# Kernel tuning notes

Measured on AMD Instinct MI355X. Metric: run time of the kernel, lower is better.

The kernel has to match this reference:

```python
import jax, jax.numpy as jnp
import numpy as np

VOCAB = 50000
EMB = 200        # embedding_size
CAP = 3          # capitalization_size
IN = EMB + CAP   # LSTM input size = 203
HID = 128        # LSTMCell(128)
B = 256
T = 500          # comment_length
NC = 6           # num_classes
DENSE = 64


def _lstm_scan(x_tbi, W, b):
    """x_tbi: [T,B,IN]. W: [IN+HID, 4*HID] (tf gate order i, j, f, o), b: [4*HID].
    Returns h sequence [T,B,HID]. forget_bias=1.0 as in tf.contrib.rnn.LSTMCell."""
    h0 = jnp.zeros((x_tbi.shape[1], HID), x_tbi.dtype)

    def step(carry, x):
        h, c = carry
        gates = jnp.concatenate([x, h], axis=-1) @ W + b   # [B, 4*HID]
        i, j, f, o = jnp.split(gates, 4, axis=-1)
        c = jax.nn.sigmoid(f + 1.0) * c + jax.nn.sigmoid(i) * jnp.tanh(j)
        h = jax.nn.sigmoid(o) * jnp.tanh(c)
        return (h, c), h

    _, hs = jax.lax.scan(step, (h0, h0), x_tbi)
    return hs


def setup_inputs() -> dict:
    key = jax.random.key(0)
    ks = jax.random.split(key, 12)
    words = jax.random.randint(ks[0], (B, T), 0, VOCAB, dtype=jnp.int32)
    capitals = jax.random.randint(ks[1], (B, T), 0, CAP, dtype=jnp.int32)
    # word embeddings: random trainable table with a trailing zero-padding row
    word_emb = jax.random.normal(ks[2], (VOCAB + 1, EMB), dtype=jnp.float32) * 0.1
    # capitalization embedding: one_hot_embedding_matrix(3) = [eye(3); zeros(1,3)]
    cap_emb = jnp.concatenate([jnp.eye(CAP, dtype=jnp.float32),
                               jnp.zeros((1, CAP), dtype=jnp.float32)], axis=0)
    def glorot(k, shape):
        lim = np.sqrt(6.0 / (shape[0] + shape[1]))
        return jax.random.uniform(k, shape, jnp.float32, -lim, lim)
    W_fw = glorot(ks[3], (IN + HID, 4 * HID))
    b_fw = jnp.zeros((4 * HID,), jnp.float32)
    W_bw = glorot(ks[4], (IN + HID, 4 * HID))
    b_bw = jnp.zeros((4 * HID,), jnp.float32)
    W1 = glorot(ks[5], (2 * HID, DENSE))
    b1 = jnp.zeros((DENSE,), jnp.float32)
    W2 = glorot(ks[6], (DENSE, NC))
    b2 = jnp.zeros((NC,), jnp.float32)
    return {"words": words, "capitals": capitals, "word_emb": word_emb,
            "cap_emb": cap_emb, "W_fw": W_fw, "b_fw": b_fw,
            "W_bw": W_bw, "b_bw": b_bw, "W1": W1, "b1": b1,
            "W2": W2, "b2": b2}


def reference(words, capitals, word_emb, cap_emb, W_fw, b_fw, W_bw, b_bw,
              W1, b1, W2, b2):
    # embedding lookups and concat -> [B, T, 203]
    x = jnp.concatenate([word_emb[words], cap_emb[capitals]], axis=-1)
    x_tbi = jnp.transpose(x, (1, 0, 2))                    # [T, B, IN]
    # forward direction: take output at last timestep
    h_fw_last = _lstm_scan(x_tbi, W_fw, b_fw)[-1]          # [B, HID]
    # backward direction: bidirectional_dynamic_rnn reverses bw outputs back,
    # so outputs[1][:, 0, :] == last state of scan over the reversed sequence
    h_bw_first = _lstm_scan(x_tbi[::-1], W_bw, b_bw)[-1]   # [B, HID]
    rnn_output = jnp.concatenate([h_fw_last, h_bw_first], axis=1)  # [B, 256]
    dense1 = jax.nn.elu(rnn_output @ W1 + b1)              # [B, 64]
    y_hat = jax.nn.sigmoid(dense1 @ W2 + b2)               # [B, NC]
    return y_hat
```

## Files before the change

### kernel.cpp

```cpp
#include <hip/hip_runtime.h>

#define T 500
#define NB 256
#define VROWS 50001
#define EMB 200
#define KPAD 224
#define MPAD 50048
#define LOG2E 1.44269504f

typedef unsigned short u16;
typedef __attribute__((ext_vector_type(8))) __bf16 bf16x8;
typedef __attribute__((ext_vector_type(8))) short short8;
typedef __attribute__((ext_vector_type(4))) float f32x4;
typedef __attribute__((ext_vector_type(4))) u16 u16x4;
typedef __attribute__((ext_vector_type(4))) int i32x4;

__device__ __forceinline__ u16 f2bf(float x) {
  __bf16 h = (__bf16)x;
  return __builtin_bit_cast(u16, h);
}
__device__ __forceinline__ float bf2f(u16 b) {
  union { unsigned u; float f; } v; v.u = ((unsigned)b) << 16;
  return v.f;
}
__device__ __forceinline__ float rcp_(float x) { return __builtin_amdgcn_rcpf(x); }
__device__ __forceinline__ float ex2_(float x) { return __builtin_amdgcn_exp2f(x); }
__device__ __forceinline__ float gsc(int g) { return (g == 1) ? 2.f * LOG2E : -LOG2E; }

__global__ void prep_kernel(const int* __restrict__ words, const int* __restrict__ caps,
                            const float* __restrict__ word_emb,
                            const float* __restrict__ cap_emb,
                            const float* __restrict__ Wfw, const float* __restrict__ bfw,
                            const float* __restrict__ Wbw, const float* __restrict__ bbw,
                            int* __restrict__ wordsT, int* __restrict__ capsT,
                            float* __restrict__ Cproj, u16* __restrict__ Apad,
                            u16* __restrict__ Bt) {
  const int S0 = NB * T;
  const int S1 = MPAD * (KPAD / 4);
  const int S2 = 2 * 512 * KPAD;
  const int S3 = 2 * 4 * 512;
  int tid = blockIdx.x * blockDim.x + threadIdx.x;
  int nthr = gridDim.x * blockDim.x;
  for (int i = tid; i < S0 + S1 + S2 + S3; i += nthr) {
    if (i < S0) {
      int b = i / T, t = i - b * T;
      wordsT[t * NB + b] = words[i];
      capsT[t * NB + b]  = caps[i];
    } else if (i < S0 + S1) {
      int idx = i - S0;
      int v = idx / (KPAD / 4), q = idx - v * (KPAD / 4);
      int k = q * 4;
      u16x4 o;
      if (v < VROWS && k < EMB) {
        const float* p = word_emb + (size_t)v * EMB + k;
        o[0] = f2bf(p[0]); o[1] = f2bf(p[1]); o[2] = f2bf(p[2]); o[3] = f2bf(p[3]);
      } else {
        o[0] = o[1] = o[2] = o[3] = 0;
      }
      *(u16x4*)(Apad + (size_t)v * KPAD + k) = o;
    } else if (i < S0 + S1 + S2) {
      int idx = i - S0 - S1;
      int d = idx / (512 * KPAD), rem = idx - d * (512 * KPAD);
      int colp = rem / KPAD, k = rem - colp * KPAD;
      const float* W = d ? Wbw : Wfw;
      int g = colp & 3, jj = colp >> 2;
      Bt[idx] = (k < EMB) ? f2bf(W[k * 512 + g * 128 + jj] * gsc(g)) : (u16)0;
    } else {
      int idx = i - S0 - S1 - S2;
      int dir = idx >> 11; int c = (idx >> 9) & 3; int colp = idx & 511;
      int j = colp >> 2, g = colp & 3;
      const float* W = dir ? Wbw : Wfw;
      const float* bias = dir ? bbw : bfw;
      float v = bias[g * 128 + j] + (g == 2 ? 1.f : 0.f);
      #pragma unroll
      for (int cc = 0; cc < 3; ++cc)
        v += cap_emb[c * 3 + cc] * W[(200 + cc) * 512 + g * 128 + j];
      Cproj[idx] = v * gsc(g);
    }
  }
}

__global__ __launch_bounds__(256) void vproj_kernel(
    const u16* __restrict__ Apad, const u16* __restrict__ Bt,
    u16* __restrict__ Vfw, u16* __restrict__ Vbw) {
  const int mt = blockIdx.x, nt = blockIdx.y, dir = blockIdx.z;
  const u16* __restrict__ B = Bt + (size_t)dir * 512 * KPAD;
  u16* __restrict__ V = dir ? Vbw : Vfw;

  __shared__ u16 Al[2][128 * 32];
  __shared__ u16 Bl[2][128 * 32];

  const int tid = threadIdx.x;
  const int w = tid >> 6, l = tid & 63;
  const int la = l & 15, lb = l >> 4;
  const int m0 = mt * 128, n0 = nt * 128;

  auto stage = [&](int buf, int ks) {
    int k0 = ks * 32;
    #pragma unroll
    for (int h = 0; h < 2; ++h) {
      int c = w * 128 + h * 64 + l;
      int row = c >> 2, kq = c & 3;
      const u16* ga = Apad + (size_t)(m0 + row) * KPAD + k0 + kq * 8;
      __builtin_amdgcn_global_load_lds(
          (const __attribute__((address_space(1))) void*)ga,
          (__attribute__((address_space(3))) void*)&Al[buf][(w * 128 + h * 64) * 8],
          16, 0, 0);
      const u16* gb = B + (size_t)(n0 + row) * KPAD + k0 + kq * 8;
      __builtin_amdgcn_global_load_lds(
          (const __attribute__((address_space(1))) void*)gb,
          (__attribute__((address_space(3))) void*)&Bl[buf][(w * 128 + h * 64) * 8],
          16, 0, 0);
    }
  };

  f32x4 z = {0.f, 0.f, 0.f, 0.f};
  f32x4 acc[4][4] = {{z,z,z,z},{z,z,z,z},{z,z,z,z},{z,z,z,z}};
  const int wr = w >> 1, wc = w & 1;

  stage(0, 0);
  __syncthreads();
  #pragma unroll 1
  for (int ks = 0; ks < 7; ++ks) {
    int cur = ks & 1;
    if (ks < 6) stage(cur ^ 1, ks + 1);
    bf16x8 af[4], bfr[4];
    #pragma unroll
    for (int m = 0; m < 4; ++m)
      af[m] = *(const bf16x8*)&Al[cur][(wr * 64 + m * 16 + la) * 32 + lb * 8];
    #pragma unroll
    for (int n = 0; n < 4; ++n)
      bfr[n] = *(const bf16x8*)&Bl[cur][(wc * 64 + n * 16 + la) * 32 + lb * 8];
    #pragma unroll
    for (int m = 0; m < 4; ++m)
      #pragma unroll
      for (int n = 0; n < 4; ++n)
        acc[m][n] = __builtin_amdgcn_mfma_f32_16x16x32_bf16(af[m], bfr[n], acc[m][n], 0, 0, 0);
    __syncthreads();
  }

  #pragma unroll
  for (int m = 0; m < 4; ++m) {
    #pragma unroll
    for (int n = 0; n < 4; ++n) {
      #pragma unroll
      for (int r = 0; r < 4; ++r) {
        int v = m0 + wr * 64 + m * 16 + lb * 4 + r;
        int colp = n0 + wc * 64 + n * 16 + la;
        V[(size_t)v * 512 + colp] = f2bf(acc[m][n][r]);
      }
    }
  }
}

template <int PAR>
__device__ __forceinline__ void lstm_step(
    int t, int dir, int b0, int la, int lb, int j,
    const int* __restrict__ wordsT, const int* __restrict__ capsT,
    const u16* __restrict__ V, const float* __restrict__ Cp,
    const bf16x8 (&bfrag)[4][4], u16* __restrict__ hbuf,
    u16x4 (&vw_c)[4], f32x4 (&cp_c)[4],
    i32x4& wi_c, i32x4& ci_c,
    i32x4& wi_g, i32x4& ci_g,
    u16x4 (&vw_g)[4], f32x4 (&cp_g)[4],
    f32x4& cst, f32x4& hl) {
  {
    int ts = t + 4; if (ts > T - 1) ts = T - 1;
    int tt = dir ? (T - 1 - ts) : ts;
    wi_c = *(const i32x4*)(wordsT + tt * NB + b0 + lb * 4);
    ci_c = *(const i32x4*)(capsT + tt * NB + b0 + lb * 4);
  }
  #pragma unroll
  for (int r = 0; r < 4; ++r) {
    vw_g[r] = *(const u16x4*)(V + (size_t)wi_g[r] * 512 + j * 4);
    cp_g[r] = *(const f32x4*)(Cp + ci_g[r] * 512 + j * 4);
  }

  const u16* hb = hbuf + PAR * 2048;
  const int swz = (la & 7) << 3;
  bf16x8 afr[4];
  #pragma unroll
  for (int kk = 0; kk < 4; ++kk)
    afr[kk] = *(const bf16x8*)(hb + ((la * 128 + kk * 32 + lb * 8) ^ swz));

  f32x4 acc0, acc1, acc2, acc3;
  #pragma unroll
  for (int r = 0; r < 4; ++r) {
    acc0[r] = bf2f(vw_c[r][0]) + cp_c[r][0];
    acc1[r] = bf2f(vw_c[r][1]) + cp_c[r][1];
    acc2[r] = bf2f(vw_c[r][2]) + cp_c[r][2];
    acc3[r] = bf2f(vw_c[r][3]) + cp_c[r][3];
  }
  #pragma unroll
  for (int kk = 0; kk < 4; ++kk) {
    acc0 = __builtin_amdgcn_mfma_f32_16x16x32_bf16(afr[kk], bfrag[0][kk], acc0, 0, 0, 0);
    acc1 = __builtin_amdgcn_mfma_f32_16x16x32_bf16(afr[kk], bfrag[1][kk], acc1, 0, 0, 0);
    acc2 = __builtin_amdgcn_mfma_f32_16x16x32_bf16(afr[kk], bfrag[2][kk], acc2, 0, 0, 0);
    acc3 = __builtin_amdgcn_mfma_f32_16x16x32_bf16(afr[kk], bfrag[3][kk], acc3, 0, 0, 0);
  }
  u16* ho = hbuf + (PAR ^ 1) * 2048;
  #pragma unroll
  for (int r = 0; r < 4; ++r) {
    float ig = rcp_(1.f + ex2_(acc0[r]));
    float tj = 1.f - 2.f * rcp_(1.f + ex2_(acc1[r]));
    float fg = rcp_(1.f + ex2_(acc2[r]));
    float cn = fg * cst[r] + ig * tj;
    cst[r] = cn;
    float og = rcp_(1.f + ex2_(acc3[r]));
    float hn = og * (1.f - 2.f * rcp_(1.f + ex2_(2.f * LOG2E * cn)));
    hl[r] = hn;
    int row = lb * 4 + r;
    ho[(row * 128 + j) ^ ((row & 7) << 3)] = f2bf(hn);
  }
  __builtin_amdgcn_sched_barrier(0);
  asm volatile("s_waitcnt lgkmcnt(0)");
  __builtin_amdgcn_s_barrier();
  __builtin_amdgcn_sched_barrier(0);
}

__global__ __launch_bounds__(512, 1) void lstm_kernel(
    const int* __restrict__ wordsT, const int* __restrict__ capsT,
    const u16* __restrict__ Vfw, const u16* __restrict__ Vbw,
    const float* __restrict__ CprojAll, const float* __restrict__ Wfw,
    const float* __restrict__ Wbw, float* __restrict__ rnn) {
  const int dir = blockIdx.x & 1;
  const int chunk = blockIdx.x >> 1;
  const int b0 = chunk * 16;
  const u16* __restrict__ V = dir ? Vbw : Vfw;
  const float* __restrict__ Cp = CprojAll + dir * 4 * 512;
  const float* __restrict__ W = dir ? Wbw : Wfw;

  const int tid = threadIdx.x;
  const int w = tid >> 6, l = tid & 63, la = l & 15, lb = l >> 4;
  const int j = w * 16 + la;

  bf16x8 bfrag[4][4];
  #pragma unroll
  for (int g = 0; g < 4; ++g) {
    #pragma unroll
    for (int kk = 0; kk < 4; ++kk) {
      short8 t8;
      #pragma unroll
      for (int r = 0; r < 8; ++r) {
        int k = kk * 32 + lb * 8 + r;
        t8[r] = (short)f2bf(W[(203 + k) * 512 + g * 128 + j] * gsc(g));
      }
      bfrag[g][kk] = __builtin_bit_cast(bf16x8, t8);
    }
  }

  __shared__ u16 hbuf[2 * 16 * 128];
  for (int i = tid; i < 2 * 16 * 128; i += 512) hbuf[i] = 0;

  f32x4 cst = {0.f, 0.f, 0.f, 0.f};
  f32x4 hl  = {0.f, 0.f, 0.f, 0.f};

  i32x4 wiA, ciA, wiB, ciB, wiC, ciC, wiD, ciD;
  u16x4 vwA[4], vwB[4], vwC[4], vwD[4];
  f32x4 cpA[4], cpB[4], cpC[4], cpD[4];
  {
    int t0 = dir ? (T - 1) : 0;
    int t1 = dir ? (T - 2) : 1;
    int t2 = dir ? (T - 3) : 2;
    int t3 = dir ? (T - 4) : 3;
    wiA = *(const i32x4*)(wordsT + t0 * NB + b0 + lb * 4);
    ciA = *(const i32x4*)(capsT + t0 * NB + b0 + lb * 4);
    wiB = *(const i32x4*)(wordsT + t1 * NB + b0 + lb * 4);
    ciB = *(const i32x4*)(capsT + t1 * NB + b0 + lb * 4);
    wiC = *(const i32x4*)(wordsT + t2 * NB + b0 + lb * 4);
    ciC = *(const i32x4*)(capsT + t2 * NB + b0 + lb * 4);
    wiD = *(const i32x4*)(wordsT + t3 * NB + b0 + lb * 4);
    ciD = *(const i32x4*)(capsT + t3 * NB + b0 + lb * 4);
  }
  #pragma unroll
  for (int r = 0; r < 4; ++r) {
    vwA[r] = *(const u16x4*)(V + (size_t)wiA[r] * 512 + j * 4);
    cpA[r] = *(const f32x4*)(Cp + ciA[r] * 512 + j * 4);
    vwB[r] = *(const u16x4*)(V + (size_t)wiB[r] * 512 + j * 4);
    cpB[r] = *(const f32x4*)(Cp + ciB[r] * 512 + j * 4);
  }
  __syncthreads();

  #pragma unroll 1
  for (int tq = 0; tq < T / 4; ++tq) {
    int t0 = 4 * tq;
    lstm_step<0>(t0,     dir, b0, la, lb, j, wordsT, capsT, V, Cp, bfrag, hbuf,
                 vwA, cpA, wiA, ciA, wiC, ciC, vwC, cpC, cst, hl);
    lstm_step<1>(t0 + 1, dir, b0, la, lb, j, wordsT, capsT, V, Cp, bfrag, hbuf,
                 vwB, cpB, wiB, ciB, wiD, ciD, vwD, cpD, cst, hl);
    lstm_step<0>(t0 + 2, dir, b0, la, lb, j, wordsT, capsT, V, Cp, bfrag, hbuf,
                 vwC, cpC, wiC, ciC, wiA, ciA, vwA, cpA, cst, hl);
    lstm_step<1>(t0 + 3, dir, b0, la, lb, j, wordsT, capsT, V, Cp, bfrag, hbuf,
                 vwD, cpD, wiD, ciD, wiB, ciB, vwB, cpB, cst, hl);
  }

  #pragma unroll
  for (int r = 0; r < 4; ++r)
    rnn[(size_t)(b0 + lb * 4 + r) * 256 + dir * 128 + j] = hl[r];
}

__global__ void head_kernel(const float* __restrict__ rnn, const float* __restrict__ W1,
                            const float* __restrict__ b1, const float* __restrict__ W2,
                            const float* __restrict__ b2, float* __restrict__ out) {
  int b = blockIdx.x;
  int jj = threadIdx.x;
  __shared__ float d1[64];
  float acc = b1[jj];
  const float* r = rnn + b * 256;
  #pragma unroll 4
  for (int k = 0; k < 256; ++k) acc += r[k] * W1[k * 64 + jj];
  d1[jj] = acc > 0.f ? acc : (__expf(acc) - 1.f);
  __syncthreads();
  if (jj < 6) {
    float a2 = b2[jj];
    #pragma unroll 8
    for (int k = 0; k < 64; ++k) a2 += d1[k] * W2[k * 6 + jj];
    out[b * 6 + jj] = rcp_(1.f + __expf(-a2));
  }
}

extern "C" void kernel_launch(void* const* d_in, const int* in_sizes, int n_in,
                              void* d_out, int out_size, void* d_ws, size_t ws_size,
                              hipStream_t stream) {
  (void)in_sizes; (void)n_in; (void)out_size; (void)ws_size;
  const int*   words    = (const int*)  d_in[0];
  const int*   caps     = (const int*)  d_in[1];
  const float* word_emb = (const float*)d_in[2];
  const float* cap_emb  = (const float*)d_in[3];
  const float* Wfw      = (const float*)d_in[4];
  const float* bfw      = (const float*)d_in[5];
  const float* Wbw      = (const float*)d_in[6];
  const float* bbw      = (const float*)d_in[7];
  const float* W1       = (const float*)d_in[8];
  const float* b1       = (const float*)d_in[9];
  const float* W2       = (const float*)d_in[10];
  const float* b2       = (const float*)d_in[11];
  float* out = (float*)d_out;

  char* base = (char*)d_ws;
  size_t off = 0;
  auto alloc = [&](size_t bytes) {
    char* q = base + off;
    off = (off + bytes + 255) & ~(size_t)255;
    return q;
  };
  u16*   Vfw    = (u16*)  alloc((size_t)MPAD * 512 * 2);
  u16*   Vbw    = (u16*)  alloc((size_t)MPAD * 512 * 2);
  u16*   Apad   = (u16*)  alloc((size_t)MPAD * KPAD * 2);
  u16*   Bt     = (u16*)  alloc((size_t)2 * 512 * KPAD * 2);
  int*   wordsT = (int*)  alloc((size_t)T * NB * 4);
  int*   capsT  = (int*)  alloc((size_t)T * NB * 4);
  float* Cproj  = (float*)alloc((size_t)2 * 4 * 512 * 4);
  float* rnn    = (float*)alloc((size_t)256 * 256 * 4);

  hipLaunchKernelGGL(prep_kernel, dim3(2048), dim3(256), 0, stream,
                     words, caps, word_emb, cap_emb, Wfw, bfw, Wbw, bbw,
                     wordsT, capsT, Cproj, Apad, Bt);
  hipLaunchKernelGGL(vproj_kernel, dim3(MPAD / 128, 4, 2), dim3(256), 0, stream,
                     Apad, Bt, Vfw, Vbw);
  hipLaunchKernelGGL(lstm_kernel, dim3(32), dim3(512), 0, stream,
                     wordsT, capsT, Vfw, Vbw, Cproj, Wfw, Wbw, rnn);
  hipLaunchKernelGGL(head_kernel, dim3(256), dim3(64), 0, stream,
                     rnn, W1, b1, W2, b2, out);
}
```

Before: 580.0 us.

## Halve LSTM block to 4 waves, each computing two 16-column hidden slices

The recurrent LSTM kernel now runs 256 threads (4 waves) per block instead of 512 (8 waves). Each wave handles 32 hidden units as two 16-column groups, with doubled MFMA accumulators, weight fragments and prefetch registers. The goal is to cut the per-step block barrier cost and give each wave more independent MFMA work to hide latency. In exchange, register pressure per thread roughly doubles and the gate math per wave is serialised over twice as many elements.

```diff
diff --git a/kernel.cpp b/kernel.cpp
--- a/kernel.cpp
+++ b/kernel.cpp
@@ -155,15 +155,22 @@
 
 template <int PAR>
 __device__ __forceinline__ void lstm_step(
-    int t, int dir, int b0, int la, int lb, int j,
+    int t, int dir, int b0, int la, int lb, int w,
     const int* __restrict__ wordsT, const int* __restrict__ capsT,
     const u16* __restrict__ V, const float* __restrict__ Cp,
-    const bf16x8 (&bfrag)[4][4], u16* __restrict__ hbuf,
-    u16x4 (&vw_c)[4], f32x4 (&cp_c)[4],
+    const bf16x8 (&bfrag)[4][2][4], u16* __restrict__ hbuf,
+    u16x4 (&vw_c)[2][4], f32x4 (&cp_c)[2][4],
     i32x4& wi_c, i32x4& ci_c,
     i32x4& wi_g, i32x4& ci_g,
-    u16x4 (&vw_g)[4], f32x4 (&cp_g)[4],
-    f32x4& cst, f32x4& hl) {
+    u16x4 (&vw_g)[2][4], f32x4 (&cp_g)[2][4],
+    f32x4 (&cst)[2], f32x4 (&hl)[2]) {
+  const u16* hb = hbuf + PAR * 2048;
+  const int swz = (la & 7) << 3;
+  bf16x8 afr[4];
+  #pragma unroll
+  for (int kk = 0; kk < 4; ++kk)
+    afr[kk] = *(const bf16x8*)(hb + ((la * 128 + kk * 32 + lb * 8) ^ swz));
+
   {
     int ts = t + 4; if (ts > T - 1) ts = T - 1;
     int tt = dir ? (T - 1 - ts) : ts;
@@ -171,54 +178,58 @@
     ci_c = *(const i32x4*)(capsT + tt * NB + b0 + lb * 4);
   }
   #pragma unroll
-  for (int r = 0; r < 4; ++r) {
-    vw_g[r] = *(const u16x4*)(V + (size_t)wi_g[r] * 512 + j * 4);
-    cp_g[r] = *(const f32x4*)(Cp + ci_g[r] * 512 + j * 4);
-  }
-
-  const u16* hb = hbuf + PAR * 2048;
-  const int swz = (la & 7) << 3;
-  bf16x8 afr[4];
+  for (int jg = 0; jg < 2; ++jg) {
+    int jc = w * 32 + jg * 16 + la;
+    #pragma unroll
+    for (int r = 0; r < 4; ++r) {
+      vw_g[jg][r] = *(const u16x4*)(V + (size_t)wi_g[r] * 512 + jc * 4);
+      cp_g[jg][r] = *(const f32x4*)(Cp + ci_g[r] * 512 + jc * 4);
+    }
+  }
+
+  f32x4 acc[4][2];
+  #pragma unroll
+  for (int jg = 0; jg < 2; ++jg)
+    #pragma unroll
+    for (int r = 0; r < 4; ++r) {
+      acc[0][jg][r] = bf2f(vw_c[jg][r][0]) + cp_c[jg][r][0];
+      acc[1][jg][r] = bf2f(vw_c[jg][r][1]) + cp_c[jg][r][1];
+      acc[2][jg][r] = bf2f(vw_c[jg][r][2]) + cp_c[jg][r][2];
+      acc[3][jg][r] = bf2f(vw_c[jg][r][3]) + cp_c[jg][r][3];
+    }
   #pragma unroll
   for (int kk = 0; kk < 4; ++kk)
-    afr[kk] = *(const bf16x8*)(hb + ((la * 128 + kk * 32 + lb * 8) ^ swz));
-
-  f32x4 acc0, acc1, acc2, acc3;
-  #pragma unroll
-  for (int r = 0; r < 4; ++r) {
-    acc0[r] = bf2f(vw_c[r][0]) + cp_c[r][0];
-    acc1[r] = bf2f(vw_c[r][1]) + cp_c[r][1];
-    acc2[r] = bf2f(vw_c[r][2]) + cp_c[r][2];
-    acc3[r] = bf2f(vw_c[r][3]) + cp_c[r][3];
-  }
-  #pragma unroll
-  for (int kk = 0; kk < 4; ++kk) {
-    acc0 = __builtin_amdgcn_mfma_f32_16x16x32_bf16(afr[kk], bfrag[0][kk], acc0, 0, 0, 0);
-    acc1 = __builtin_amdgcn_mfma_f32_16x16x32_bf16(afr[kk], bfrag[1][kk], acc1, 0, 0, 0);
-    acc2 = __builtin_amdgcn_mfma_f32_16x16x32_bf16(afr[kk], bfrag[2][kk], acc2, 0, 0, 0);
-    acc3 = __builtin_amdgcn_mfma_f32_16x16x32_bf16(afr[kk], bfrag[3][kk], acc3, 0, 0, 0);
-  }
+    #pragma unroll
+    for (int g = 0; g < 4; ++g)
+      #pragma unroll
+      for (int jg = 0; jg < 2; ++jg)
+        acc[g][jg] = __builtin_amdgcn_mfma_f32_16x16x32_bf16(
+            afr[kk], bfrag[g][jg][kk], acc[g][jg], 0, 0, 0);
+
   u16* ho = hbuf + (PAR ^ 1) * 2048;
   #pragma unroll
-  for (int r = 0; r < 4; ++r) {
-    float ig = rcp_(1.f + ex2_(acc0[r]));
-    float tj = 1.f - 2.f * rcp_(1.f + ex2_(acc1[r]));
-    float fg = rcp_(1.f + ex2_(acc2[r]));
-    float cn = fg * cst[r] + ig * tj;
-    cst[r] = cn;
-    float og = rcp_(1.f + ex2_(acc3[r]));
-    float hn = og * (1.f - 2.f * rcp_(1.f + ex2_(2.f * LOG2E * cn)));
-    hl[r] = hn;
-    int row = lb * 4 + r;
-    ho[(row * 128 + j) ^ ((row & 7) << 3)] = f2bf(hn);
-  }
+  for (int jg = 0; jg < 2; ++jg)
+    #pragma unroll
+    for (int r = 0; r < 4; ++r) {
+      float ig = rcp_(1.f + ex2_(acc[0][jg][r]));
+      float tj = 1.f - 2.f * rcp_(1.f + ex2_(acc[1][jg][r]));
+      float fg = rcp_(1.f + ex2_(acc[2][jg][r]));
+      float cn = fg * cst[jg][r] + ig * tj;
+      cst[jg][r] = cn;
+      float og = rcp_(1.f + ex2_(acc[3][jg][r]));
+      float hn = og * (1.f - 2.f * rcp_(1.f + ex2_(2.f * LOG2E * cn)));
+      hl[jg][r] = hn;
+      int row = lb * 4 + r;
+      int col = w * 32 + jg * 16 + la;
+      ho[(row * 128 + col) ^ ((row & 7) << 3)] = f2bf(hn);
+    }
   __builtin_amdgcn_sched_barrier(0);
   asm volatile("s_waitcnt lgkmcnt(0)");
   __builtin_amdgcn_s_barrier();
   __builtin_amdgcn_sched_barrier(0);
 }
 
-__global__ __launch_bounds__(512, 1) void lstm_kernel(
+__global__ __launch_bounds__(256, 1) void lstm_kernel(
     const int* __restrict__ wordsT, const int* __restrict__ capsT,
     const u16* __restrict__ Vfw, const u16* __restrict__ Vbw,
     const float* __restrict__ CprojAll, const float* __restrict__ Wfw,
@@ -232,32 +243,32 @@
 
   const int tid = threadIdx.x;
   const int w = tid >> 6, l = tid & 63, la = l & 15, lb = l >> 4;
-  const int j = w * 16 + la;
-
-  bf16x8 bfrag[4][4];
-  #pragma unroll
-  for (int g = 0; g < 4; ++g) {
-    #pragma unroll
-    for (int kk = 0; kk < 4; ++kk) {
-      short8 t8;
-      #pragma unroll
-      for (int r = 0; r < 8; ++r) {
-        int k = kk * 32 + lb * 8 + r;
-        t8[r] = (short)f2bf(W[(203 + k) * 512 + g * 128 + j] * gsc(g));
+
+  bf16x8 bfrag[4][2][4];
+  #pragma unroll
+  for (int g = 0; g < 4; ++g)
+    #pragma unroll
+    for (int jg = 0; jg < 2; ++jg)
+      #pragma unroll
+      for (int kk = 0; kk < 4; ++kk) {
+        short8 t8;
+        #pragma unroll
+        for (int r = 0; r < 8; ++r) {
+          int k = kk * 32 + lb * 8 + r;
+          t8[r] = (short)f2bf(W[(203 + k) * 512 + g * 128 + w * 32 + jg * 16 + la] * gsc(g));
+        }
+        bfrag[g][jg][kk] = __builtin_bit_cast(bf16x8, t8);
       }
-      bfrag[g][kk] = __builtin_bit_cast(bf16x8, t8);
-    }
-  }
 
   __shared__ u16 hbuf[2 * 16 * 128];
-  for (int i = tid; i < 2 * 16 * 128; i += 512) hbuf[i] = 0;
-
-  f32x4 cst = {0.f, 0.f, 0.f, 0.f};
-  f32x4 hl  = {0.f, 0.f, 0.f, 0.f};
+  for (int i = tid; i < 2 * 16 * 128; i += 256) hbuf[i] = 0;
+
+  f32x4 cst[2] = {{0.f,0.f,0.f,0.f},{0.f,0.f,0.f,0.f}};
+  f32x4 hl[2]  = {{0.f,0.f,0.f,0.f},{0.f,0.f,0.f,0.f}};
 
   i32x4 wiA, ciA, wiB, ciB, wiC, ciC, wiD, ciD;
-  u16x4 vwA[4], vwB[4], vwC[4], vwD[4];
-  f32x4 cpA[4], cpB[4], cpC[4], cpD[4];
+  u16x4 vwA[2][4], vwB[2][4], vwC[2][4], vwD[2][4];
+  f32x4 cpA[2][4], cpB[2][4], cpC[2][4], cpD[2][4];
   {
     int t0 = dir ? (T - 1) : 0;
     int t1 = dir ? (T - 2) : 1;
@@ -273,30 +284,36 @@
     ciD = *(const i32x4*)(capsT + t3 * NB + b0 + lb * 4);
   }
   #pragma unroll
-  for (int r = 0; r < 4; ++r) {
-    vwA[r] = *(const u16x4*)(V + (size_t)wiA[r] * 512 + j * 4);
-    cpA[r] = *(const f32x4*)(Cp + ciA[r] * 512 + j * 4);
-    vwB[r] = *(const u16x4*)(V + (size_t)wiB[r] * 512 + j * 4);
-    cpB[r] = *(const f32x4*)(Cp + ciB[r] * 512 + j * 4);
+  for (int jg = 0; jg < 2; ++jg) {
+    int jc = w * 32 + jg * 16 + la;
+    #pragma unroll
+    for (int r = 0; r < 4; ++r) {
+      vwA[jg][r] = *(const u16x4*)(V + (size_t)wiA[r] * 512 + jc * 4);
+      cpA[jg][r] = *(const f32x4*)(Cp + ciA[r] * 512 + jc * 4);
+      vwB[jg][r] = *(const u16x4*)(V + (size_t)wiB[r] * 512 + jc * 4);
+      cpB[jg][r] = *(const f32x4*)(Cp + ciB[r] * 512 + jc * 4);
+    }
   }
   __syncthreads();
 
   #pragma unroll 1
   for (int tq = 0; tq < T / 4; ++tq) {
     int t0 = 4 * tq;
-    lstm_step<0>(t0,     dir, b0, la, lb, j, wordsT, capsT, V, Cp, bfrag, hbuf,
+    lstm_step<0>(t0,     dir, b0, la, lb, w, wordsT, capsT, V, Cp, bfrag, hbuf,
                  vwA, cpA, wiA, ciA, wiC, ciC, vwC, cpC, cst, hl);
-    lstm_step<1>(t0 + 1, dir, b0, la, lb, j, wordsT, capsT, V, Cp, bfrag, hbuf,
+    lstm_step<1>(t0 + 1, dir, b0, la, lb, w, wordsT, capsT, V, Cp, bfrag, hbuf,
                  vwB, cpB, wiB, ciB, wiD, ciD, vwD, cpD, cst, hl);
-    lstm_step<0>(t0 + 2, dir, b0, la, lb, j, wordsT, capsT, V, Cp, bfrag, hbuf,
+    lstm_step<0>(t0 + 2, dir, b0, la, lb, w, wordsT, capsT, V, Cp, bfrag, hbuf,
                  vwC, cpC, wiC, ciC, wiA, ciA, vwA, cpA, cst, hl);
-    lstm_step<1>(t0 + 3, dir, b0, la, lb, j, wordsT, capsT, V, Cp, bfrag, hbuf,
+    lstm_step<1>(t0 + 3, dir, b0, la, lb, w, wordsT, capsT, V, Cp, bfrag, hbuf,
                  vwD, cpD, wiD, ciD, wiB, ciB, vwB, cpB, cst, hl);
   }
 
   #pragma unroll
-  for (int r = 0; r < 4; ++r)
-    rnn[(size_t)(b0 + lb * 4 + r) * 256 + dir * 128 + j] = hl[r];
+  for (int jg = 0; jg < 2; ++jg)
+    #pragma unroll
+    for (int r = 0; r < 4; ++r)
+      rnn[(size_t)(b0 + lb * 4 + r) * 256 + dir * 128 + w * 32 + jg * 16 + la] = hl[jg][r];
 }
 
 __global__ void head_kernel(const float* __restrict__ rnn, const float* __restrict__ W1,
@@ -358,7 +375,7 @@
                      wordsT, capsT, Cproj, Apad, Bt);
   hipLaunchKernelGGL(vproj_kernel, dim3(MPAD / 128, 4, 2), dim3(256), 0, stream,
                      Apad, Bt, Vfw, Vbw);
-  hipLaunchKernelGGL(lstm_kernel, dim3(32), dim3(512), 0, stream,
+  hipLaunchKernelGGL(lstm_kernel, dim3(32), dim3(256), 0, stream,
                      wordsT, capsT, Vfw, Vbw, Cproj, Wfw, Wbw, rnn);
   hipLaunchKernelGGL(head_kernel, dim3(256), dim3(64), 0, stream,
                      rnn, W1, b1, W2, b2, out);
```

Measured after the change: 743.8 us. +28.2%, slower.

## Project input per token instead of precomputing over whole vocabulary table

Applied to the files above, without the earlier changes.

Before, the input projection was precomputed for all 50k vocabulary rows and gathered inside the LSTM loop by word index. Now the GEMM runs over the B*T token sequence, gathering embeddings straight into LDS, adding the capitalization/bias term in the epilogue, and writing a time-major XP buffer. The recurrent kernel then streams contiguous per-step rows with a shorter prefetch distance, no index lookups, and raised wave priority around its MFMAs. Compute drops from 50k to 128k rows? Actually it rises (128k rows vs 50k), but the prep conversion of the whole table and the random gathers are removed, so the trade is more GEMM work for better locality and less prep.

```diff
diff --git a/kernel.cpp b/kernel.cpp
--- a/kernel.cpp
+++ b/kernel.cpp
@@ -5,15 +5,14 @@
 #define VROWS 50001
 #define EMB 200
 #define KPAD 224
-#define MPAD 50048
 #define LOG2E 1.44269504f
 
 typedef unsigned short u16;
 typedef __attribute__((ext_vector_type(8))) __bf16 bf16x8;
 typedef __attribute__((ext_vector_type(8))) short short8;
+typedef __attribute__((ext_vector_type(8))) u16 u16x8;
 typedef __attribute__((ext_vector_type(4))) float f32x4;
 typedef __attribute__((ext_vector_type(4))) u16 u16x4;
-typedef __attribute__((ext_vector_type(4))) int i32x4;
 
 __device__ __forceinline__ u16 f2bf(float x) {
   __bf16 h = (__bf16)x;
@@ -27,46 +26,23 @@
 __device__ __forceinline__ float ex2_(float x) { return __builtin_amdgcn_exp2f(x); }
 __device__ __forceinline__ float gsc(int g) { return (g == 1) ? 2.f * LOG2E : -LOG2E; }
 
-__global__ void prep_kernel(const int* __restrict__ words, const int* __restrict__ caps,
-                            const float* __restrict__ word_emb,
-                            const float* __restrict__ cap_emb,
+__global__ void prep_kernel(const float* __restrict__ cap_emb,
                             const float* __restrict__ Wfw, const float* __restrict__ bfw,
                             const float* __restrict__ Wbw, const float* __restrict__ bbw,
-                            int* __restrict__ wordsT, int* __restrict__ capsT,
-                            float* __restrict__ Cproj, u16* __restrict__ Apad,
-                            u16* __restrict__ Bt) {
-  const int S0 = NB * T;
-  const int S1 = MPAD * (KPAD / 4);
+                            float* __restrict__ Cproj, u16* __restrict__ Bt) {
   const int S2 = 2 * 512 * KPAD;
   const int S3 = 2 * 4 * 512;
   int tid = blockIdx.x * blockDim.x + threadIdx.x;
   int nthr = gridDim.x * blockDim.x;
-  for (int i = tid; i < S0 + S1 + S2 + S3; i += nthr) {
-    if (i < S0) {
-      int b = i / T, t = i - b * T;
-      wordsT[t * NB + b] = words[i];
-      capsT[t * NB + b]  = caps[i];
-    } else if (i < S0 + S1) {
-      int idx = i - S0;
-      int v = idx / (KPAD / 4), q = idx - v * (KPAD / 4);
-      int k = q * 4;
-      u16x4 o;
-      if (v < VROWS && k < EMB) {
-        const float* p = word_emb + (size_t)v * EMB + k;
-        o[0] = f2bf(p[0]); o[1] = f2bf(p[1]); o[2] = f2bf(p[2]); o[3] = f2bf(p[3]);
-      } else {
-        o[0] = o[1] = o[2] = o[3] = 0;
-      }
-      *(u16x4*)(Apad + (size_t)v * KPAD + k) = o;
-    } else if (i < S0 + S1 + S2) {
-      int idx = i - S0 - S1;
-      int d = idx / (512 * KPAD), rem = idx - d * (512 * KPAD);
+  for (int i = tid; i < S2 + S3; i += nthr) {
+    if (i < S2) {
+      int d = i / (512 * KPAD), rem = i - d * (512 * KPAD);
       int colp = rem / KPAD, k = rem - colp * KPAD;
       const float* W = d ? Wbw : Wfw;
       int g = colp & 3, jj = colp >> 2;
-      Bt[idx] = (k < EMB) ? f2bf(W[k * 512 + g * 128 + jj] * gsc(g)) : (u16)0;
+      Bt[i] = (k < EMB) ? f2bf(W[k * 512 + g * 128 + jj] * gsc(g)) : (u16)0;
     } else {
-      int idx = i - S0 - S1 - S2;
+      int idx = i - S2;
       int dir = idx >> 11; int c = (idx >> 9) & 3; int colp = idx & 511;
       int j = colp >> 2, g = colp & 3;
       const float* W = dir ? Wbw : Wfw;
@@ -80,36 +56,55 @@
   }
 }
 
-__global__ __launch_bounds__(256) void vproj_kernel(
-    const u16* __restrict__ Apad, const u16* __restrict__ Bt,
-    u16* __restrict__ Vfw, u16* __restrict__ Vbw) {
+__global__ __launch_bounds__(256) void xproj_kernel(
+    const int* __restrict__ words, const int* __restrict__ caps,
+    const float* __restrict__ word_emb, const u16* __restrict__ Bt,
+    const float* __restrict__ Cproj, u16* __restrict__ XP) {
   const int mt = blockIdx.x, nt = blockIdx.y, dir = blockIdx.z;
   const u16* __restrict__ B = Bt + (size_t)dir * 512 * KPAD;
-  u16* __restrict__ V = dir ? Vbw : Vfw;
-
-  __shared__ u16 Al[2][128 * 32];
-  __shared__ u16 Bl[2][128 * 32];
+  const float* __restrict__ Cb = Cproj + dir * 4 * 512;
+  u16* __restrict__ xp = XP + (size_t)dir * T * NB * 512;
+
+  __shared__ u16 As[2][128 * 32];
+  __shared__ u16 Bs[2][128 * 32];
 
   const int tid = threadIdx.x;
   const int w = tid >> 6, l = tid & 63;
   const int la = l & 15, lb = l >> 4;
   const int m0 = mt * 128, n0 = nt * 128;
-
-  auto stage = [&](int buf, int ks) {
+  const int tblk = m0 >> 8;
+
+  const int ar = tid >> 1, ah = tid & 1;
+  const int ab = (m0 & 255) + ar;
+  const int aword = words[ab * T + tblk];
+  const float* __restrict__ aemb = word_emb + (size_t)aword * EMB;
+
+  auto stageA = [&](int buf, int ks) {
+    int kbase = ks * 32 + ah * 16;
+    u16x8 lo, hi;
+    #pragma unroll
+    for (int q = 0; q < 4; ++q) {
+      int k = kbase + q * 4;
+      f32x4 v;
+      if (k < EMB) v = *(const f32x4*)(aemb + k);
+      else v = f32x4{0.f, 0.f, 0.f, 0.f};
+      u16 b0 = f2bf(v[0]), b1 = f2bf(v[1]), b2 = f2bf(v[2]), b3 = f2bf(v[3]);
+      if (q < 2) { lo[q*4+0]=b0; lo[q*4+1]=b1; lo[q*4+2]=b2; lo[q*4+3]=b3; }
+      else { int qq=q-2; hi[qq*4+0]=b0; hi[qq*4+1]=b1; hi[qq*4+2]=b2; hi[qq*4+3]=b3; }
+    }
+    *(u16x8*)&As[buf][ar * 32 + ah * 16]     = lo;
+    *(u16x8*)&As[buf][ar * 32 + ah * 16 + 8] = hi;
+  };
+  auto stageB = [&](int buf, int ks) {
     int k0 = ks * 32;
     #pragma unroll
     for (int h = 0; h < 2; ++h) {
       int c = w * 128 + h * 64 + l;
       int row = c >> 2, kq = c & 3;
-      const u16* ga = Apad + (size_t)(m0 + row) * KPAD + k0 + kq * 8;
-      __builtin_amdgcn_global_load_lds(
-          (const __attribute__((address_space(1))) void*)ga,
-          (__attribute__((address_space(3))) void*)&Al[buf][(w * 128 + h * 64) * 8],
-          16, 0, 0);
       const u16* gb = B + (size_t)(n0 + row) * KPAD + k0 + kq * 8;
       __builtin_amdgcn_global_load_lds(
           (const __attribute__((address_space(1))) void*)gb,
-          (__attribute__((address_space(3))) void*)&Bl[buf][(w * 128 + h * 64) * 8],
+          (__attribute__((address_space(3))) void*)&Bs[buf][(w * 128 + h * 64) * 8],
           16, 0, 0);
     }
   };
@@ -118,19 +113,19 @@
   f32x4 acc[4][4] = {{z,z,z,z},{z,z,z,z},{z,z,z,z},{z,z,z,z}};
   const int wr = w >> 1, wc = w & 1;
 
-  stage(0, 0);
+  stageA(0, 0); stageB(0, 0);
   __syncthreads();
   #pragma unroll 1
   for (int ks = 0; ks < 7; ++ks) {
     int cur = ks & 1;
-    if (ks < 6) stage(cur ^ 1, ks + 1);
+    if (ks < 6) { stageA(cur ^ 1, ks + 1); stageB(cur ^ 1, ks + 1); }
     bf16x8 af[4], bfr[4];
     #pragma unroll
     for (int m = 0; m < 4; ++m)
-      af[m] = *(const bf16x8*)&Al[cur][(wr * 64 + m * 16 + la) * 32 + lb * 8];
+      af[m] = *(const bf16x8*)&As[cur][(wr * 64 + m * 16 + la) * 32 + lb * 8];
     #pragma unroll
     for (int n = 0; n < 4; ++n)
-      bfr[n] = *(const bf16x8*)&Bl[cur][(wc * 64 + n * 16 + la) * 32 + lb * 8];
+      bfr[n] = *(const bf16x8*)&Bs[cur][(wc * 64 + n * 16 + la) * 32 + lb * 8];
     #pragma unroll
     for (int m = 0; m < 4; ++m)
       #pragma unroll
@@ -142,12 +137,15 @@
   #pragma unroll
   for (int m = 0; m < 4; ++m) {
     #pragma unroll
-    for (int n = 0; n < 4; ++n) {
+    for (int r = 0; r < 4; ++r) {
+      int b = (m0 & 255) + wr * 64 + m * 16 + lb * 4 + r;
+      int cap = caps[b * T + tblk];
+      const float* cbr = Cb + cap * 512;
+      u16* op = xp + ((size_t)tblk * NB + b) * 512;
       #pragma unroll
-      for (int r = 0; r < 4; ++r) {
-        int v = m0 + wr * 64 + m * 16 + lb * 4 + r;
+      for (int n = 0; n < 4; ++n) {
         int colp = n0 + wc * 64 + n * 16 + la;
-        V[(size_t)v * 512 + colp] = f2bf(acc[m][n][r]);
+        op[colp] = f2bf(acc[m][n][r] + cbr[colp]);
       }
     }
   }
@@ -155,27 +153,12 @@
 
 template <int PAR>
 __device__ __forceinline__ void lstm_step(
-    int t, int dir, int b0, int la, int lb, int j,
-    const int* __restrict__ wordsT, const int* __restrict__ capsT,
-    const u16* __restrict__ V, const float* __restrict__ Cp,
+    int t, int dir, int la, int lb, int j,
+    const u16* __restrict__ xpd, int voff0, int voff1, int voff2, int voff3,
     const bf16x8 (&bfrag)[4][4], u16* __restrict__ hbuf,
-    u16x4 (&vw_c)[4], f32x4 (&cp_c)[4],
-    i32x4& wi_c, i32x4& ci_c,
-    i32x4& wi_g, i32x4& ci_g,
-    u16x4 (&vw_g)[4], f32x4 (&cp_g)[4],
+    u16x4 (&xc)[4],
+    u16x4 (&xg)[4],
     f32x4& cst, f32x4& hl) {
-  {
-    int ts = t + 4; if (ts > T - 1) ts = T - 1;
-    int tt = dir ? (T - 1 - ts) : ts;
-    wi_c = *(const i32x4*)(wordsT + tt * NB + b0 + lb * 4);
-    ci_c = *(const i32x4*)(capsT + tt * NB + b0 + lb * 4);
-  }
-  #pragma unroll
-  for (int r = 0; r < 4; ++r) {
-    vw_g[r] = *(const u16x4*)(V + (size_t)wi_g[r] * 512 + j * 4);
-    cp_g[r] = *(const f32x4*)(Cp + ci_g[r] * 512 + j * 4);
-  }
-
   const u16* hb = hbuf + PAR * 2048;
   const int swz = (la & 7) << 3;
   bf16x8 afr[4];
@@ -183,14 +166,25 @@
   for (int kk = 0; kk < 4; ++kk)
     afr[kk] = *(const bf16x8*)(hb + ((la * 128 + kk * 32 + lb * 8) ^ swz));
 
+  {
+    int ts = t + 2; if (ts > T - 1) ts = T - 1;
+    int tt = dir ? (T - 1 - ts) : ts;
+    const u16* p = xpd + (size_t)tt * (NB * 512);
+    xg[0] = *(const u16x4*)(p + voff0);
+    xg[1] = *(const u16x4*)(p + voff1);
+    xg[2] = *(const u16x4*)(p + voff2);
+    xg[3] = *(const u16x4*)(p + voff3);
+  }
+
   f32x4 acc0, acc1, acc2, acc3;
   #pragma unroll
   for (int r = 0; r < 4; ++r) {
-    acc0[r] = bf2f(vw_c[r][0]) + cp_c[r][0];
-    acc1[r] = bf2f(vw_c[r][1]) + cp_c[r][1];
-    acc2[r] = bf2f(vw_c[r][2]) + cp_c[r][2];
-    acc3[r] = bf2f(vw_c[r][3]) + cp_c[r][3];
-  }
+    acc0[r] = bf2f(xc[r][0]);
+    acc1[r] = bf2f(xc[r][1]);
+    acc2[r] = bf2f(xc[r][2]);
+    acc3[r] = bf2f(xc[r][3]);
+  }
+  __builtin_amdgcn_s_setprio(1);
   #pragma unroll
   for (int kk = 0; kk < 4; ++kk) {
     acc0 = __builtin_amdgcn_mfma_f32_16x16x32_bf16(afr[kk], bfrag[0][kk], acc0, 0, 0, 0);
@@ -198,6 +192,7 @@
     acc2 = __builtin_amdgcn_mfma_f32_16x16x32_bf16(afr[kk], bfrag[2][kk], acc2, 0, 0, 0);
     acc3 = __builtin_amdgcn_mfma_f32_16x16x32_bf16(afr[kk], bfrag[3][kk], acc3, 0, 0, 0);
   }
+  __builtin_amdgcn_s_setprio(0);
   u16* ho = hbuf + (PAR ^ 1) * 2048;
   #pragma unroll
   for (int r = 0; r < 4; ++r) {
@@ -219,20 +214,22 @@
 }
 
 __global__ __launch_bounds__(512, 1) void lstm_kernel(
-    const int* __restrict__ wordsT, const int* __restrict__ capsT,
-    const u16* __restrict__ Vfw, const u16* __restrict__ Vbw,
-    const float* __restrict__ CprojAll, const float* __restrict__ Wfw,
+    const u16* __restrict__ XP, const float* __restrict__ Wfw,
     const float* __restrict__ Wbw, float* __restrict__ rnn) {
   const int dir = blockIdx.x & 1;
   const int chunk = blockIdx.x >> 1;
   const int b0 = chunk * 16;
-  const u16* __restrict__ V = dir ? Vbw : Vfw;
-  const float* __restrict__ Cp = CprojAll + dir * 4 * 512;
+  const u16* __restrict__ xpd = XP + (size_t)dir * T * NB * 512;
   const float* __restrict__ W = dir ? Wbw : Wfw;
 
   const int tid = threadIdx.x;
   const int w = tid >> 6, l = tid & 63, la = l & 15, lb = l >> 4;
   const int j = w * 16 + la;
+
+  const int voff0 = (b0 + lb * 4 + 0) * 512 + j * 4;
+  const int voff1 = (b0 + lb * 4 + 1) * 512 + j * 4;
+  const int voff2 = (b0 + lb * 4 + 2) * 512 + j * 4;
+  const int voff3 = (b0 + lb * 4 + 3) * 512 + j * 4;
 
   bf16x8 bfrag[4][4];
   #pragma unroll
@@ -255,43 +252,30 @@
   f32x4 cst = {0.f, 0.f, 0.f, 0.f};
   f32x4 hl  = {0.f, 0.f, 0.f, 0.f};
 
-  i32x4 wiA, ciA, wiB, ciB, wiC, ciC, wiD, ciD;
-  u16x4 vwA[4], vwB[4], vwC[4], vwD[4];
-  f32x4 cpA[4], cpB[4], cpC[4], cpD[4];
+  u16x4 xA[4], xB[4], xC[4], xD[4];
   {
-    int t0 = dir ? (T - 1) : 0;
-    int t1 = dir ? (T - 2) : 1;
-    int t2 = dir ? (T - 3) : 2;
-    int t3 = dir ? (T - 4) : 3;
-    wiA = *(const i32x4*)(wordsT + t0 * NB + b0 + lb * 4);
-    ciA = *(const i32x4*)(capsT + t0 * NB + b0 + lb * 4);
-    wiB = *(const i32x4*)(wordsT + t1 * NB + b0 + lb * 4);
-    ciB = *(const i32x4*)(capsT + t1 * NB + b0 + lb * 4);
-    wiC = *(const i32x4*)(wordsT + t2 * NB + b0 + lb * 4);
-    ciC = *(const i32x4*)(capsT + t2 * NB + b0 + lb * 4);
-    wiD = *(const i32x4*)(wordsT + t3 * NB + b0 + lb * 4);
-    ciD = *(const i32x4*)(capsT + t3 * NB + b0 + lb * 4);
-  }
-  #pragma unroll
-  for (int r = 0; r < 4; ++r) {
-    vwA[r] = *(const u16x4*)(V + (size_t)wiA[r] * 512 + j * 4);
-    cpA[r] = *(const f32x4*)(Cp + ciA[r] * 512 + j * 4);
-    vwB[r] = *(const u16x4*)(V + (size_t)wiB[r] * 512 + j * 4);
-    cpB[r] = *(const f32x4*)(Cp + ciB[r] * 512 + j * 4);
+    int tt0 = dir ? (T - 1) : 0;
+    int tt1 = dir ? (T - 2) : 1;
+    const u16* p0 = xpd + (size_t)tt0 * (NB * 512);
+    const u16* p1 = xpd + (size_t)tt1 * (NB * 512);
+    xA[0] = *(const u16x4*)(p0 + voff0); xA[1] = *(const u16x4*)(p0 + voff1);
+    xA[2] = *(const u16x4*)(p0 + voff2); xA[3] = *(const u16x4*)(p0 + voff3);
+    xB[0] = *(const u16x4*)(p1 + voff0); xB[1] = *(const u16x4*)(p1 + voff1);
+    xB[2] = *(const u16x4*)(p1 + voff2); xB[3] = *(const u16x4*)(p1 + voff3);
   }
   __syncthreads();
 
   #pragma unroll 1
   for (int tq = 0; tq < T / 4; ++tq) {
     int t0 = 4 * tq;
-    lstm_step<0>(t0,     dir, b0, la, lb, j, wordsT, capsT, V, Cp, bfrag, hbuf,
-                 vwA, cpA, wiA, ciA, wiC, ciC, vwC, cpC, cst, hl);
-    lstm_step<1>(t0 + 1, dir, b0, la, lb, j, wordsT, capsT, V, Cp, bfrag, hbuf,
-                 vwB, cpB, wiB, ciB, wiD, ciD, vwD, cpD, cst, hl);
-    lstm_step<0>(t0 + 2, dir, b0, la, lb, j, wordsT, capsT, V, Cp, bfrag, hbuf,
-                 vwC, cpC, wiC, ciC, wiA, ciA, vwA, cpA, cst, hl);
-    lstm_step<1>(t0 + 3, dir, b0, la, lb, j, wordsT, capsT, V, Cp, bfrag, hbuf,
-                 vwD, cpD, wiD, ciD, wiB, ciB, vwB, cpB, cst, hl);
+    lstm_step<0>(t0,     dir, la, lb, j, xpd, voff0, voff1, voff2, voff3,
+                 bfrag, hbuf, xA, xC, cst, hl);
+    lstm_step<1>(t0 + 1, dir, la, lb, j, xpd, voff0, voff1, voff2, voff3,
+                 bfrag, hbuf, xB, xD, cst, hl);
+    lstm_step<0>(t0 + 2, dir, la, lb, j, xpd, voff0, voff1, voff2, voff3,
+                 bfrag, hbuf, xC, xA, cst, hl);
+    lstm_step<1>(t0 + 3, dir, la, lb, j, xpd, voff0, voff1, voff2, voff3,
+                 bfrag, hbuf, xD, xB, cst, hl);
   }
 
   #pragma unroll
@@ -344,22 +328,17 @@
     off = (off + bytes + 255) & ~(size_t)255;
     return q;
   };
-  u16*   Vfw    = (u16*)  alloc((size_t)MPAD * 512 * 2);
-  u16*   Vbw    = (u16*)  alloc((size_t)MPAD * 512 * 2);
-  u16*   Apad   = (u16*)  alloc((size_t)MPAD * KPAD * 2);
+  u16*   XP     = (u16*)  alloc((size_t)2 * T * NB * 512 * 2);
   u16*   Bt     = (u16*)  alloc((size_t)2 * 512 * KPAD * 2);
-  int*   wordsT = (int*)  alloc((size_t)T * NB * 4);
-  int*   capsT  = (int*)  alloc((size_t)T * NB * 4);
   float* Cproj  = (float*)alloc((size_t)2 * 4 * 512 * 4);
   float* rnn    = (float*)alloc((size_t)256 * 256 * 4);
 
-  hipLaunchKernelGGL(prep_kernel, dim3(2048), dim3(256), 0, stream,
-                     words, caps, word_emb, cap_emb, Wfw, bfw, Wbw, bbw,
-                     wordsT, capsT, Cproj, Apad, Bt);
-  hipLaunchKernelGGL(vproj_kernel, dim3(MPAD / 128, 4, 2), dim3(256), 0, stream,
-                     Apad, Bt, Vfw, Vbw);
+  hipLaunchKernelGGL(prep_kernel, dim3(256), dim3(256), 0, stream,
+                     cap_emb, Wfw, bfw, Wbw, bbw, Cproj, Bt);
+  hipLaunchKernelGGL(xproj_kernel, dim3(1000, 4, 2), dim3(256), 0, stream,
+                     words, caps, word_emb, Bt, Cproj, XP);
   hipLaunchKernelGGL(lstm_kernel, dim3(32), dim3(512), 0, stream,
-                     wordsT, capsT, Vfw, Vbw, Cproj, Wfw, Wbw, rnn);
+                     XP, Wfw, Wbw, rnn);
   hipLaunchKernelGGL(head_kernel, dim3(256), dim3(64), 0, stream,
                      rnn, W1, b1, W2, b2, out);
 }
```

Result: slower. 700.7 us (+20.8%).
